# Kernel tuning notes

Hardware: AMD Instinct MI355X
Metric: run time of the kernel (lower is better)

Reference implementation:

```python
import jax, jax.numpy as jnp
import numpy as np

MLOG32 = float(np.log(32.0))


def _maxpool(x, k):
    # F.max_pool2d(stride=1, padding=k//2) pads with -inf, matching init value
    pad = k // 2
    return jax.lax.reduce_window(x, -jnp.inf, jax.lax.max, (1, 1, k, k), (1, 1, 1, 1),
                                 ((0, 0), (0, 0), (pad, pad), (pad, pad)))


def _minpool(x, k):
    return -_maxpool(-x, k)


def _local_sum(x, k):
    # conv2d with all-ones kxk kernel, zero padding, same spatial size
    pad = k // 2
    return jax.lax.reduce_window(x, 0.0, jax.lax.add, (1, 1, k, k), (1, 1, 1, 1),
                                 ((0, 0), (0, 0), (pad, pad), (pad, pad)))


def _conv3(x, kern):
    # torch conv2d == cross-correlation == lax conv (no kernel flip)
    return jax.lax.conv_general_dilated(x, kern, (1, 1), ((1, 1), (1, 1)),
                                        dimension_numbers=('NCHW', 'OIHW', 'NCHW'))


def _otsu(gray, bins=32):
    # vectorized per-batch Otsu threshold; gray in [0,1]
    B, _, H, W = gray.shape
    v = gray.reshape(B, -1)
    idx = jnp.clip((v * bins).astype(jnp.int32), 0, bins - 1)  # histc semantics, v==1 -> last bin
    hist = jax.vmap(lambda i: jnp.bincount(i, length=bins))(idx).astype(gray.dtype)
    p = hist / (H * W + 1e-6)
    xs = jnp.linspace(0.0, 1.0, bins, dtype=gray.dtype)
    omega = jnp.cumsum(p, axis=1)
    mu = jnp.cumsum(p * xs[None, :], axis=1)
    mu_t = mu[:, -1:]
    sigma_b2 = (mu_t * omega - mu) ** 2 / (omega * (1.0 - omega) + 1e-8)
    kbest = jnp.argmax(sigma_b2, axis=1)
    edges = jnp.linspace(0.0, 1.0, bins + 1, dtype=gray.dtype)
    return edges[kbest].reshape(B, 1, 1, 1)


def _concept_maps(image_rgb, cell_dilate=10, k_local=9):
    r, g, b = image_rgb[:, 0:1], image_rgb[:, 1:2], image_rgb[:, 2:3]
    gray = jnp.clip(0.5 * (0.299 * r + 0.587 * g + 0.114 * b + 1.0), 0.0, 1.0)
    thr = _otsu(gray)
    nuc = (gray <= thr).astype(gray.dtype)
    # morphological open+close, k=3
    e = _minpool(nuc, 3)
    d = _maxpool(e, 3)
    d = _maxpool(d, 3)
    e2 = _minpool(d, 3)
    nuc = (e2 > 0.5).astype(gray.dtype)
    er = _minpool(nuc, 3)
    boundary = jnp.maximum(nuc - er, 0.0)
    lap_k = jnp.array([[0, 1, 0], [1, -4, 1], [0, 1, 0]], dtype=gray.dtype).reshape(1, 1, 3, 3)
    lap = jnp.abs(_conv3(nuc, lap_k))
    den = _local_sum(boundary, 5) + 1e-6
    roughness = lap * boundary / den
    kx = jnp.array([[1, 0, -1], [2, 0, -2], [1, 0, -1]], dtype=gray.dtype).reshape(1, 1, 3, 3)
    ky = jnp.array([[1, 2, 1], [0, 0, 0], [-1, -2, -1]], dtype=gray.dtype).reshape(1, 1, 3, 3)
    gx = _conv3(gray, kx)
    gy = _conv3(gray, ky)
    ang = jnp.arctan2(gy, gx)
    den_orient = _local_sum(jnp.ones_like(gray), k_local) + 1e-6
    ms = _local_sum(jnp.sin(ang), k_local) / den_orient
    mc = _local_sum(jnp.cos(ang), k_local) / den_orient
    circ_var = 1.0 - jnp.sqrt(ms ** 2 + mc ** 2 + 1e-6)
    kd = cell_dilate if cell_dilate % 2 == 1 else cell_dilate + 1  # force odd
    cell = jnp.minimum(_maxpool(nuc, kd), 1.0)
    A_n = _local_sum(nuc, k_local)
    A_c = jnp.maximum(_local_sum(cell, k_local) - A_n, 1.0)
    nc = A_n / A_c
    g2 = _local_sum(gray * gray, k_local) / den_orient
    g1 = _local_sum(gray, k_local) / den_orient
    ent_like = jnp.log1p(jnp.maximum(g2 - g1 * g1, 0.0))
    z_maps = jnp.concatenate([roughness, circ_var, nc, ent_like], axis=1)
    return z_maps, nuc


def _energy_forward(image_rgb, cal_a, cal_b, alpha_logits, tau_p, Ht, Wt):
    z_maps, nuc = _concept_maps(image_rgb)
    z0 = jnp.log1p(jnp.maximum(z_maps[:, 0:1], 0.0))
    z1 = jnp.clip(z_maps[:, 1:2], 0.0, 1.0)
    z2 = jnp.log1p(jnp.maximum(z_maps[:, 2:3], 0.0))
    z3 = jnp.clip(z_maps[:, 3:4], 0.0, MLOG32)
    z_stable = jnp.concatenate([z0, z1, z2, z3], axis=1)
    z_cal = jax.nn.softplus(cal_a)[None, :, None, None] * z_stable + cal_b[None, :, None, None]
    alpha = jax.nn.softmax(alpha_logits)[None, :, None, None]
    E = jnp.sum(alpha * z_cal, axis=1, keepdims=True)
    B = E.shape[0]
    if (E.shape[2], E.shape[3]) != (Ht, Wt):
        E_t = jax.image.resize(E, (B, 1, Ht, Wt), method='linear')
    else:
        E_t = E
    tau = 0.2 + jax.nn.softplus(tau_p)
    A = jax.nn.softmax((-E_t / tau).reshape(B, 1, Ht * Wt), axis=-1).reshape(B, 1, Ht, Wt)
    return A, z_maps, nuc, E_t


def setup_inputs() -> dict:
    key = jax.random.key(0)
    k1, k2, k3, k4 = jax.random.split(key, 4)
    B, H, W = 16, 512, 512
    image_rgb = 2.0 * jax.random.uniform(k1, (B, 3, H, W), dtype=jnp.float32) - 1.0
    cal_a = 1.0 + 0.1 * jax.random.normal(k2, (4,), jnp.float32)
    cal_b = 0.1 * jax.random.normal(k3, (4,), jnp.float32)
    alpha_logits = 0.1 * jax.random.normal(k4, (4,), jnp.float32)
    tau_p = jnp.float32(0.5)
    return {"image_rgb": image_rgb, "cal_a": cal_a, "cal_b": cal_b,
            "alpha_logits": alpha_logits, "tau_p": tau_p, "target_h": 512, "target_w": 512}


def reference(image_rgb, cal_a, cal_b, alpha_logits, tau_p, target_h, target_w):
    return _energy_forward(image_rgb, cal_a, cal_b, alpha_logits, tau_p, int(target_h), int(target_w))
```

## Files before the change

kernel.cpp:

```cpp
#include <hip/hip_runtime.h>
#include <math.h>
#include <stdint.h>

#define HW 512
#define IMG (HW*HW)
#define GS 49
#define MLOG32f 3.4657359027997265f
#define WFENCE() __asm__ __volatile__("" ::: "memory")

__device__ __forceinline__ float grayf(float r, float g, float b) {
    float t = __fadd_rn(__fadd_rn(__fmul_rn(0.299f, r), __fmul_rn(0.587f, g)), __fmul_rn(0.114f, b));
    float s = __fmul_rn(0.5f, __fadd_rn(t, 1.0f));
    return fminf(fmaxf(s, 0.0f), 1.0f);
}

__device__ __forceinline__ float softplusf(float x) {
    return fmaxf(x, 0.0f) + log1pf(expf(-fabsf(x)));
}

__device__ __forceinline__ float frcp(float x)  { return __builtin_amdgcn_rcpf(x); }
__device__ __forceinline__ float frsq(float x)  { return __builtin_amdgcn_rsqf(x); }
__device__ __forceinline__ float flog1p(float x){ return __logf(1.0f + x); }

__device__ __forceinline__ uint64_t kmask(int lo, int hi) {
    return (1ull << hi) - (1ull << lo);
}

__global__ __launch_bounds__(256) void k_gray_hist(const float* __restrict__ img,
                                                   float* __restrict__ gray,
                                                   int* __restrict__ hist) {
    __shared__ int lh[32];
    int tid = threadIdx.x;
    int b = blockIdx.y;
    if (tid < 32) lh[tid] = 0;
    __syncthreads();
    const float4* rp = (const float4*)(img + (size_t)b * 3 * IMG);
    const float4* gp = (const float4*)(img + (size_t)b * 3 * IMG + IMG);
    const float4* bp = (const float4*)(img + (size_t)b * 3 * IMG + 2 * IMG);
    float4* op = (float4*)(gray + (size_t)b * IMG);
    int i = blockIdx.x * 256 + tid;
    float4 r = rp[i], g = gp[i], bb = bp[i];
    float4 o;
    o.x = grayf(r.x, g.x, bb.x);
    o.y = grayf(r.y, g.y, bb.y);
    o.z = grayf(r.z, g.z, bb.z);
    o.w = grayf(r.w, g.w, bb.w);
    op[i] = o;
    int idx[4];
    idx[0] = min(max((int)(o.x * 32.0f), 0), 31);
    idx[1] = min(max((int)(o.y * 32.0f), 0), 31);
    idx[2] = min(max((int)(o.z * 32.0f), 0), 31);
    idx[3] = min(max((int)(o.w * 32.0f), 0), 31);
    int lane = tid & 63;
    int bin = lane & 31;
    int cnt = 0;
    #pragma unroll
    for (int e = 0; e < 4; e++) {
        int v = idx[e];
        unsigned long long m0 = __ballot((v & 1)  != 0);
        unsigned long long m1 = __ballot((v & 2)  != 0);
        unsigned long long m2 = __ballot((v & 4)  != 0);
        unsigned long long m3 = __ballot((v & 8)  != 0);
        unsigned long long m4 = __ballot((v & 16) != 0);
        unsigned long long mm = (bin & 1)  ? m0 : ~m0;
        mm &= (bin & 2)  ? m1 : ~m1;
        mm &= (bin & 4)  ? m2 : ~m2;
        mm &= (bin & 8)  ? m3 : ~m3;
        mm &= (bin & 16) ? m4 : ~m4;
        cnt += __popcll(mm);
    }
    if (lane < 32) atomicAdd(&lh[bin], cnt);
    __syncthreads();
    if (tid < 32) atomicAdd(&hist[b * 32 + tid], lh[tid]);
}

__global__ void k_otsu_sc(const int* __restrict__ hist,
                          const float* __restrict__ cal_a, const float* __restrict__ cal_b,
                          const float* __restrict__ alpha_logits, const float* __restrict__ tau_p,
                          float* __restrict__ thr, float* __restrict__ sc, int B) {
    int tid = threadIdx.x;
    if (tid < B) {
        const int* h = hist + tid * 32;
        float omega[32], mu[32];
        float co = 0.0f, cm = 0.0f;
        for (int k = 0; k < 32; k++) {
            float pk = (float)h[k] * (1.0f / 262144.0f);
            float xs = (float)((double)k / 31.0);
            co += pk;
            cm += pk * xs;
            omega[k] = co; mu[k] = cm;
        }
        float mu_t = mu[31];
        float best = -1e30f; int kb = 0;
        for (int k = 0; k < 32; k++) {
            float t = mu_t * omega[k] - mu[k];
            float sb = (t * t) / (omega[k] * (1.0f - omega[k]) + 1e-8f);
            if (sb > best) { best = sb; kb = k; }
        }
        thr[tid] = (float)kb * 0.03125f;
    }
    if (tid == 63) {
        float al[4];
        float m = -1e30f;
        for (int c = 0; c < 4; c++) { al[c] = alpha_logits[c]; m = fmaxf(m, al[c]); }
        float e[4]; float s = 0.0f;
        for (int c = 0; c < 4; c++) { e[c] = expf(al[c] - m); s += e[c]; }
        float bias = 0.0f;
        for (int c = 0; c < 4; c++) {
            float alpha = e[c] / s;
            sc[c] = alpha * softplusf(cal_a[c]);
            bias += alpha * cal_b[c];
        }
        sc[4] = bias;
        float tau = 0.2f + softplusf(tau_p[0]);
        sc[5] = tau;
        sc[6] = -1.0f / tau;
    }
}

__global__ __launch_bounds__(256) void k_thresh(const float* __restrict__ gray,
                                                const float* __restrict__ thr,
                                                uint32_t* __restrict__ packed) {
    int b = blockIdx.y;
    int i = blockIdx.x * 256 + threadIdx.x;
    float t = thr[b];
    float v = gray[(size_t)b * IMG + i];
    unsigned long long m = __ballot(v <= t);
    if ((threadIdx.x & 63) == 0)
        *(uint64_t*)&packed[(size_t)b * 8192 + (i >> 5)] = m;
}

__global__ __launch_bounds__(256, 5) void k_maps(const float* __restrict__ gray,
                                              const uint32_t* __restrict__ p0,
                                              float* __restrict__ zmap,
                                              float* __restrict__ nucf,
                                              float* __restrict__ Eout,
                                              const float* __restrict__ sc,
                                              float* __restrict__ expsum) {
    __shared__ __align__(16) char smem[30248];
    float*    gt   = (float*)smem;
    float2*   rsP1 = (float2*)(smem + 8232);
    float2*   rsP2 = (float2*)(smem + 18728);
    uint64_t* m0   = (uint64_t*)(smem + 8232);
    uint64_t* m1   = m0 + 58;
    uint64_t* dilh = m1 + 58;
    uint64_t* ehr  = dilh + 50;
    uint64_t* nrow = (uint64_t*)(smem + 29224);
    uint64_t* bnd  = nrow + 50;
    uint64_t* cell = bnd + 36;
    int*      rs_nPT = (int*)smem;
    int*      rs_cPT = (int*)(smem + 1408);
    int*      rs_bPT = (int*)(smem + 2816);
    float*    red  = (float*)(smem + 30232);

    int tid = threadIdx.x, b = blockIdx.z;
    int x0 = blockIdx.x * 32, y0 = blockIdx.y * 32;
    int w0 = x0 >> 5;
    const float* gb = gray + (size_t)b * IMG;
    const uint32_t* pb = p0 + (size_t)b * 8192;

    if (tid >= 64) {
        for (int s = tid - 64; s < 504; s += 192) {
            int r = s / 12, c4 = s - r * 12;
            int gy = y0 + r - 5;
            int gxf = (x0 >> 2) + c4 - 2;
            float4 v = make_float4(0.f, 0.f, 0.f, 0.f);
            if ((unsigned)gy < (unsigned)HW && (unsigned)gxf < 128u)
                v = *(const float4*)(gb + gy * HW + (gxf << 2));
            float* dst = &gt[r * GS + (c4 << 2)];
            dst[0] = v.x; dst[1] = v.y; dst[2] = v.z; dst[3] = v.w;
        }
    } else {
        int ml = tid;
        uint64_t mcol = ~0ull;
        if (x0 == 0)   mcol &= ~((1ull << 13) - 1);
        if (x0 == 480) mcol = (1ull << 45) - 1;
        if (ml < 58) {
            int gy = y0 - 13 + ml;
            uint64_t v = 0;
            if ((unsigned)gy < (unsigned)HW) {
                const uint32_t* rowp = pb + gy * 16;
                uint64_t wm = (w0 > 0)  ? rowp[w0 - 1] : 0;
                uint64_t wc = rowp[w0];
                uint64_t wp = (w0 < 15) ? rowp[w0 + 1] : 0;
                v = (wm >> 19) | (wc << 13) | (wp << 45);
            }
            m0[ml] = v;
        }
        WFENCE();
        if (ml >= 1 && ml < 57) {
            uint64_t e = ~0ull;
            #pragma unroll
            for (int dt = -1; dt <= 1; dt++) {
                int q = ml + dt;
                int gy = y0 - 13 + q;
                uint64_t vv = ((unsigned)gy < (unsigned)HW) ? (m0[q] | ~mcol) : ~0ull;
                e &= vv & (vv << 1) & (vv >> 1);
            }
            m1[ml] = e;
        }
        WFENCE();
        if (ml >= 2 && ml < 56) {
            uint64_t d = 0;
            #pragma unroll
            for (int dt = -1; dt <= 1; dt++) {
                int q = ml + dt;
                int gy = y0 - 13 + q;
                uint64_t vv = ((unsigned)gy < (unsigned)HW) ? (m1[q] & mcol) : 0;
                d |= vv | (vv << 1) | (vv >> 1);
            }
            m0[ml] = d;
        }
        WFENCE();
        if (ml >= 3 && ml < 55) {
            uint64_t d = 0;
            #pragma unroll
            for (int dt = -1; dt <= 1; dt++) {
                int q = ml + dt;
                int gy = y0 - 13 + q;
                uint64_t vv = ((unsigned)gy < (unsigned)HW) ? (m0[q] & mcol) : 0;
                d |= vv | (vv << 1) | (vv >> 1);
            }
            m1[ml] = d;
        }
        WFENCE();
        if (ml >= 4 && ml < 54) {
            uint64_t e = ~0ull;
            #pragma unroll
            for (int dt = -1; dt <= 1; dt++) {
                int q = ml + dt;
                int gy = y0 - 13 + q;
                uint64_t vv = ((unsigned)gy < (unsigned)HW) ? (m1[q] | ~mcol) : ~0ull;
                e &= vv & (vv << 1) & (vv >> 1);
            }
            m0[ml] = e;
        }
        WFENCE();
        if (ml < 50) {
            int gy = y0 - 9 + ml;
            uint64_t v = 0;
            if ((unsigned)gy < (unsigned)HW)
                v = ((m0[ml + 4] & mcol) >> 4) & ((1ull << 50) - 1);
            nrow[ml] = v;
        }
        WFENCE();
        uint64_t mwin = kmask(x0 == 0 ? 9 : 0, x0 == 480 ? 41 : 50);
        if (ml < 50) {
            uint64_t v = nrow[ml];
            uint64_t d = v | (v << 1) | (v >> 1);
            d = d | (d << 2) | (d >> 2);
            d = d | (d << 2) | (d >> 2);
            dilh[ml] = d;
        }
        if (ml >= 6 && ml < 44) {
            int y = y0 - 9 + ml;
            uint64_t m = ((unsigned)y < (unsigned)HW) ? mwin : 0;
            uint64_t v = nrow[ml] | ~m;
            ehr[ml] = v & (v << 1) & (v >> 1);
        }
        WFENCE();
        if (ml < 36) {
            int r = ml + 7;
            uint64_t er = ehr[r - 1] & ehr[r] & ehr[r + 1];
            bnd[ml] = nrow[r] & ~er;
        }
        if (ml < 40) {
            int r = ml + 5;
            int y = y0 - 4 + ml;
            uint64_t c = 0;
            #pragma unroll
            for (int d = -5; d <= 5; d++) c |= dilh[r + d];
            uint64_t m = ((unsigned)y < (unsigned)HW) ? mwin : 0;
            cell[ml] = c & m;
        }
    }
    __syncthreads();

    for (int i = tid; i < 320; i += 256) {
        int ly = i >> 3, c0 = (i & 7) << 2;
        int gyb = y0 + ly - 4;
        bool rowok = (unsigned)gyb < (unsigned)HW;
        int gx0 = x0 + c0 - 4;
        int base = ly * GS + c0 + 3;
        float a0p = gt[base],          a1p = gt[base + GS],          a2p = gt[base + 2 * GS];
        float a0q = gt[base + 1],      a1q = gt[base + GS + 1],      a2q = gt[base + 2 * GS + 1];
        float sa[12], ca[12], v[12];
        #pragma unroll
        for (int j = 0; j < 12; j++) {
            float a0r = gt[base + 2 + j], a1r = gt[base + GS + 2 + j], a2r = gt[base + 2 * GS + 2 + j];
            v[j] = a1q;
            float s = 0.0f, c = 0.0f;
            if (rowok && (unsigned)(gx0 + j) < (unsigned)HW) {
                float gxv = (a0p - a0r) + 2.0f * (a1p - a1r) + (a2p - a2r);
                float gyv = (a0p + 2.0f * a0q + a0r) - (a2p + 2.0f * a2q + a2r);
                float r2 = gxv * gxv + gyv * gyv;
                if (r2 > 0.0f) { float ir = frsq(r2); s = gyv * ir; c = gxv * ir; }
                else { s = 0.0f; c = 1.0f; }
            }
            sa[j] = s; ca[j] = c;
            a0p = a0q; a1p = a1q; a2p = a2q;
            a0q = a0r; a1q = a1r; a2q = a2r;
        }
        float ss = sa[0]+sa[1]+sa[2]+sa[3]+sa[4]+sa[5]+sa[6]+sa[7]+sa[8];
        float cs = ca[0]+ca[1]+ca[2]+ca[3]+ca[4]+ca[5]+ca[6]+ca[7]+ca[8];
        float gs = v[0]+v[1]+v[2]+v[3]+v[4]+v[5]+v[6]+v[7]+v[8];
        float g2 = v[0]*v[0]+v[1]*v[1]+v[2]*v[2]+v[3]*v[3]+v[4]*v[4]+v[5]*v[5]+v[6]*v[6]+v[7]*v[7]+v[8]*v[8];
        #pragma unroll
        for (int q = 0; q < 4; q++) {
            float2 t1; t1.x = ss; t1.y = cs;
            float2 t2; t2.x = gs; t2.y = g2;
            rsP1[(c0 + q) * 41 + ly] = t1;
            rsP2[(c0 + q) * 41 + ly] = t2;
            if (q < 3) {
                ss += sa[9 + q] - sa[q]; cs += ca[9 + q] - ca[q];
                gs += v[9 + q] - v[q];
                g2 += v[9 + q] * v[9 + q] - v[q] * v[q];
            }
        }
    }
    __syncthreads();

    int p = tid & 31, py0 = (tid >> 5) << 2;
    int gx = x0 + p;
    float cntx = (float)(min(gx + 4, HW - 1) - max(gx - 4, 0) + 1);
    float z1v[4], z3v[4];
    {
        float2 v[12];
        #pragma unroll
        for (int j = 0; j < 12; j++) v[j] = rsP1[p * 41 + py0 + j];
        float ss = v[0].x+v[1].x+v[2].x+v[3].x+v[4].x+v[5].x+v[6].x+v[7].x+v[8].x;
        float cs = v[0].y+v[1].y+v[2].y+v[3].y+v[4].y+v[5].y+v[6].y+v[7].y+v[8].y;
        #pragma unroll
        for (int q = 0; q < 4; q++) {
            int gy = y0 + py0 + q;
            float cnty = (float)(min(gy + 4, HW - 1) - max(gy - 4, 0) + 1);
            float iden = frcp(cnty * cntx + 1e-6f);
            float ms = ss * iden, mc = cs * iden;
            z1v[q] = 1.0f - sqrtf(ms * ms + mc * mc + 1e-6f);
            if (q < 3) { ss += v[9 + q].x - v[q].x; cs += v[9 + q].y - v[q].y; }
        }
    }
    {
        float2 v[12];
        #pragma unroll
        for (int j = 0; j < 12; j++) v[j] = rsP2[p * 41 + py0 + j];
        float gs = v[0].x+v[1].x+v[2].x+v[3].x+v[4].x+v[5].x+v[6].x+v[7].x+v[8].x;
        float g2 = v[0].y+v[1].y+v[2].y+v[3].y+v[4].y+v[5].y+v[6].y+v[7].y+v[8].y;
        #pragma unroll
        for (int q = 0; q < 4; q++) {
            int gy = y0 + py0 + q;
            float cnty = (float)(min(gy + 4, HW - 1) - max(gy - 4, 0) + 1);
            float iden = frcp(cnty * cntx + 1e-6f);
            float g1 = gs * iden, gq = g2 * iden;
            z3v[q] = flog1p(fmaxf(gq - g1 * g1, 0.0f));
            if (q < 3) { gs += v[9 + q].x - v[q].x; g2 += v[9 + q].y - v[q].y; }
        }
    }
    for (int i = tid; i < 320; i += 256) {
        int rr = i >> 3, p8 = i & 7, pbase = p8 << 2;
        uint64_t rn = nrow[rr + 5], rc = cell[rr];
        int vn = 0, vc = 0;
        #pragma unroll
        for (int e = 0; e < 4; e++) {
            int pp = pbase + e;
            vn |= __popcll((rn >> (pp + 5)) & 0x1FFull) << (e * 8);
            vc |= __popcll((rc >> (pp + 5)) & 0x1FFull) << (e * 8);
        }
        rs_nPT[p8 * 44 + rr] = vn;
        rs_cPT[p8 * 44 + rr] = vc;
    }
    for (int i = tid; i < 288; i += 256) {
        int rr = i >> 3, p8 = i & 7, pbase = p8 << 2;
        uint64_t rb = bnd[rr];
        int vb = 0;
        #pragma unroll
        for (int e = 0; e < 4; e++) {
            int pp = pbase + e;
            vb |= __popcll((rb >> (pp + 7)) & 0x1Full) << (e * 8);
        }
        rs_bPT[p8 * 40 + rr] = vb;
    }
    __syncthreads();

    float w0f = sc[0], w1f = sc[1], w2f = sc[2], w3f = sc[3], bias = sc[4], ntau = sc[6];
    float* z0p = zmap + ((size_t)b * 4 + 0) * IMG;
    float* z1p = zmap + ((size_t)b * 4 + 1) * IMG;
    float* z2p = zmap + ((size_t)b * 4 + 2) * IMG;
    float* z3p = zmap + ((size_t)b * 4 + 3) * IMG;
    float* Ep  = Eout + (size_t)b * IMG;
    float* np  = nucf + (size_t)b * IMG;
    float acc = 0.0f;
    {
        int p8 = p >> 2, sh = (p & 3) << 3;
        int4 na = *(const int4*)&rs_nPT[p8 * 44 + py0];
        int4 nb = *(const int4*)&rs_nPT[p8 * 44 + py0 + 4];
        int4 nc = *(const int4*)&rs_nPT[p8 * 44 + py0 + 8];
        int4 ka = *(const int4*)&rs_cPT[p8 * 44 + py0];
        int4 kb = *(const int4*)&rs_cPT[p8 * 44 + py0 + 4];
        int4 kc = *(const int4*)&rs_cPT[p8 * 44 + py0 + 8];
        int4 ba = *(const int4*)&rs_bPT[p8 * 40 + py0];
        int4 bbv = *(const int4*)&rs_bPT[p8 * 40 + py0 + 4];
        int en[12], ec[12], eb[8];
        en[0]=na.x; en[1]=na.y; en[2]=na.z; en[3]=na.w;
        en[4]=nb.x; en[5]=nb.y; en[6]=nb.z; en[7]=nb.w;
        en[8]=nc.x; en[9]=nc.y; en[10]=nc.z; en[11]=nc.w;
        ec[0]=ka.x; ec[1]=ka.y; ec[2]=ka.z; ec[3]=ka.w;
        ec[4]=kb.x; ec[5]=kb.y; ec[6]=kb.z; ec[7]=kb.w;
        ec[8]=kc.x; ec[9]=kc.y; ec[10]=kc.z; ec[11]=kc.w;
        eb[0]=ba.x; eb[1]=ba.y; eb[2]=ba.z; eb[3]=ba.w;
        eb[4]=bbv.x; eb[5]=bbv.y; eb[6]=bbv.z; eb[7]=bbv.w;
        #pragma unroll
        for (int j = 0; j < 12; j++) { en[j] = (en[j] >> sh) & 0xFF; ec[j] = (ec[j] >> sh) & 0xFF; }
        #pragma unroll
        for (int j = 0; j < 8; j++) eb[j] = (eb[j] >> sh) & 0xFF;
        int An = en[0]+en[1]+en[2]+en[3]+en[4]+en[5]+en[6]+en[7]+en[8];
        int Ac = ec[0]+ec[1]+ec[2]+ec[3]+ec[4]+ec[5]+ec[6]+ec[7]+ec[8];
        int db = eb[0]+eb[1]+eb[2]+eb[3]+eb[4];
        int kk = p + 9;
        #pragma unroll
        for (int q = 0; q < 4; q++) {
            int py = py0 + q;
            int r = py + 9;
            uint64_t rowc = nrow[r];
            int cbit = (int)((rowc >> kk) & 1);
            int nb4  = (int)((nrow[r - 1] >> kk) & 1) + (int)((nrow[r + 1] >> kk) & 1)
                     + (int)((rowc >> (kk - 1)) & 1) + (int)((rowc >> (kk + 1)) & 1);
            int lap = nb4 - 4 * cbit; lap = lap < 0 ? -lap : lap;
            int bc  = (int)((bnd[py + 2] >> kk) & 1);
            float rough = (float)(lap * bc) * frcp((float)db + 1e-6f);
            float z2 = (float)An * frcp(fmaxf((float)(Ac - An), 1.0f));
            float z0s = flog1p(fmaxf(rough, 0.0f));
            float z1s = fminf(fmaxf(z1v[q], 0.0f), 1.0f);
            float z2s = flog1p(fmaxf(z2, 0.0f));
            float z3s = fminf(fmaxf(z3v[q], 0.0f), MLOG32f);
            float E = w0f * z0s + w1f * z1s + w2f * z2s + w3f * z3s + bias;
            int gy = y0 + py;
            size_t o = (size_t)gy * HW + x0 + p;
            z0p[o] = rough;
            z1p[o] = z1v[q];
            z2p[o] = z2;
            z3p[o] = z3v[q];
            Ep[o]  = E;
            np[o]  = (float)cbit;
            acc += __expf(E * ntau);
            if (q < 3) {
                An += en[9 + q] - en[q];
                Ac += ec[9 + q] - ec[q];
                db += eb[5 + q] - eb[q];
            }
        }
    }
    for (int off = 32; off > 0; off >>= 1) acc += __shfl_down(acc, off, 64);
    if ((tid & 63) == 0) red[tid >> 6] = acc;
    __syncthreads();
    if (tid == 0) atomicAdd(&expsum[b], red[0] + red[1] + red[2] + red[3]);
}

__global__ __launch_bounds__(256) void k_softmaxA(const float* __restrict__ E,
                                                  float* __restrict__ A,
                                                  const float* __restrict__ sc,
                                                  const float* __restrict__ expsum) {
    int b = blockIdx.y;
    int i = blockIdx.x * 256 + threadIdx.x;
    float ntau = sc[6];
    float invS = 1.0f / expsum[b];
    const float4* Ep = (const float4*)(E + (size_t)b * IMG);
    float4* Ap = (float4*)(A + (size_t)b * IMG);
    float4 e = Ep[i];
    float4 o;
    o.x = __expf(e.x * ntau) * invS;
    o.y = __expf(e.y * ntau) * invS;
    o.z = __expf(e.z * ntau) * invS;
    o.w = __expf(e.w * ntau) * invS;
    Ap[i] = o;
}

extern "C" void kernel_launch(void* const* d_in, const int* in_sizes, int n_in,
                              void* d_out, int out_size, void* d_ws, size_t ws_size,
                              hipStream_t stream) {
    const float* img   = (const float*)d_in[0];
    const float* cal_a = (const float*)d_in[1];
    const float* cal_b = (const float*)d_in[2];
    const float* alpha = (const float*)d_in[3];
    const float* tau_p = (const float*)d_in[4];
    int B = in_sizes[0] / (3 * IMG);

    float* out  = (float*)d_out;
    float* A    = out;
    float* zmap = out + (size_t)B * IMG;
    float* nuc  = out + (size_t)B * IMG * 5;
    float* E    = out + (size_t)B * IMG * 6;
    float* gray = A;

    int*      hist    = (int*)d_ws;
    float*    expsum  = (float*)d_ws + B * 32;
    float*    thr     = expsum + B;
    float*    sc      = thr + B;
    uint32_t* packed0 = (uint32_t*)d_ws + 1024;

    hipMemsetAsync(d_ws, 0, (size_t)(B * 32 + B) * 4, stream);
    k_gray_hist<<<dim3(IMG / 1024, B), 256, 0, stream>>>(img, gray, hist);
    k_otsu_sc<<<1, 64, 0, stream>>>(hist, cal_a, cal_b, alpha, tau_p, thr, sc, B);
    k_thresh<<<dim3(IMG / 256, B), 256, 0, stream>>>(gray, thr, packed0);
    dim3 tg(HW / 32, HW / 32, B);
    k_maps<<<tg, 256, 0, stream>>>(gray, packed0, zmap, nuc, E, sc, expsum);
    k_softmaxA<<<dim3(IMG / 1024, B), 256, 0, stream>>>(E, A, sc, expsum);
}
```

Baseline: 240.0 us.

## Shrink k_maps shared memory by aliasing buffers and computing popcounts per thread

The Sobel pass now keeps the gray-sum partials in registers and writes them to a buffer that aliases the gray tile once a barrier has passed, which cuts the shared-memory footprint. The packed popcount tables in shared memory are replaced by per-thread popcount computation straight from the bitmask rows, removing a pass and a barrier. Launch bounds rise from 5 to 7 blocks per SM to take advantage of the lower LDS use. The cost is an extra barrier, more registers held across it, and redundant popcount work per thread.

```diff
diff --git a/kernel.cpp b/kernel.cpp
--- a/kernel.cpp
+++ b/kernel.cpp
@@ -130,28 +130,69 @@
         *(uint64_t*)&packed[(size_t)b * 8192 + (i >> 5)] = m;
 }
 
-__global__ __launch_bounds__(256, 5) void k_maps(const float* __restrict__ gray,
+__device__ __forceinline__ void sobel_item(const float* __restrict__ gt, float2* __restrict__ rsP1,
+                                           int i, int x0, int y0,
+                                           float* __restrict__ hgs, float* __restrict__ hg2) {
+    int ly = i >> 3, c0 = (i & 7) << 2;
+    int gyb = y0 + ly - 4;
+    bool rowok = (unsigned)gyb < (unsigned)HW;
+    int gx0 = x0 + c0 - 4;
+    int base = ly * GS + c0 + 3;
+    float a0p = gt[base],          a1p = gt[base + GS],          a2p = gt[base + 2 * GS];
+    float a0q = gt[base + 1],      a1q = gt[base + GS + 1],      a2q = gt[base + 2 * GS + 1];
+    float sa[12], ca[12], v[12];
+    #pragma unroll
+    for (int j = 0; j < 12; j++) {
+        float a0r = gt[base + 2 + j], a1r = gt[base + GS + 2 + j], a2r = gt[base + 2 * GS + 2 + j];
+        v[j] = a1q;
+        float s = 0.0f, c = 0.0f;
+        if (rowok && (unsigned)(gx0 + j) < (unsigned)HW) {
+            float gxv = (a0p - a0r) + 2.0f * (a1p - a1r) + (a2p - a2r);
+            float gyv = (a0p + 2.0f * a0q + a0r) - (a2p + 2.0f * a2q + a2r);
+            float r2 = gxv * gxv + gyv * gyv;
+            if (r2 > 0.0f) { float ir = frsq(r2); s = gyv * ir; c = gxv * ir; }
+            else { s = 0.0f; c = 1.0f; }
+        }
+        sa[j] = s; ca[j] = c;
+        a0p = a0q; a1p = a1q; a2p = a2q;
+        a0q = a0r; a1q = a1r; a2q = a2r;
+    }
+    float ss = sa[0]+sa[1]+sa[2]+sa[3]+sa[4]+sa[5]+sa[6]+sa[7]+sa[8];
+    float cs = ca[0]+ca[1]+ca[2]+ca[3]+ca[4]+ca[5]+ca[6]+ca[7]+ca[8];
+    float gs = v[0]+v[1]+v[2]+v[3]+v[4]+v[5]+v[6]+v[7]+v[8];
+    float g2 = v[0]*v[0]+v[1]*v[1]+v[2]*v[2]+v[3]*v[3]+v[4]*v[4]+v[5]*v[5]+v[6]*v[6]+v[7]*v[7]+v[8]*v[8];
+    #pragma unroll
+    for (int q = 0; q < 4; q++) {
+        float2 t1; t1.x = ss; t1.y = cs;
+        rsP1[(c0 + q) * 41 + ly] = t1;
+        hgs[q] = gs; hg2[q] = g2;
+        if (q < 3) {
+            ss += sa[9 + q] - sa[q]; cs += ca[9 + q] - ca[q];
+            gs += v[9 + q] - v[q];
+            g2 += v[9 + q] * v[9 + q] - v[q] * v[q];
+        }
+    }
+}
+
+__global__ __launch_bounds__(256, 7) void k_maps(const float* __restrict__ gray,
                                               const uint32_t* __restrict__ p0,
                                               float* __restrict__ zmap,
                                               float* __restrict__ nucf,
                                               float* __restrict__ Eout,
                                               const float* __restrict__ sc,
                                               float* __restrict__ expsum) {
-    __shared__ __align__(16) char smem[30248];
+    __shared__ __align__(16) char smem[22016];
     float*    gt   = (float*)smem;
-    float2*   rsP1 = (float2*)(smem + 8232);
-    float2*   rsP2 = (float2*)(smem + 18728);
-    uint64_t* m0   = (uint64_t*)(smem + 8232);
+    float2*   rsP2 = (float2*)smem;
+    float2*   rsP1 = (float2*)(smem + 10496);
+    uint64_t* m0   = (uint64_t*)(smem + 10496);
     uint64_t* m1   = m0 + 58;
     uint64_t* dilh = m1 + 58;
     uint64_t* ehr  = dilh + 50;
-    uint64_t* nrow = (uint64_t*)(smem + 29224);
+    uint64_t* nrow = (uint64_t*)(smem + 20992);
     uint64_t* bnd  = nrow + 50;
     uint64_t* cell = bnd + 36;
-    int*      rs_nPT = (int*)smem;
-    int*      rs_cPT = (int*)(smem + 1408);
-    int*      rs_bPT = (int*)(smem + 2816);
-    float*    red  = (float*)(smem + 30232);
+    float*    red  = (float*)(smem + 22000);
 
     int tid = threadIdx.x, b = blockIdx.z;
     int x0 = blockIdx.x * 32, y0 = blockIdx.y * 32;
@@ -276,46 +317,25 @@
     }
     __syncthreads();
 
-    for (int i = tid; i < 320; i += 256) {
-        int ly = i >> 3, c0 = (i & 7) << 2;
-        int gyb = y0 + ly - 4;
-        bool rowok = (unsigned)gyb < (unsigned)HW;
-        int gx0 = x0 + c0 - 4;
-        int base = ly * GS + c0 + 3;
-        float a0p = gt[base],          a1p = gt[base + GS],          a2p = gt[base + 2 * GS];
-        float a0q = gt[base + 1],      a1q = gt[base + GS + 1],      a2q = gt[base + 2 * GS + 1];
-        float sa[12], ca[12], v[12];
-        #pragma unroll
-        for (int j = 0; j < 12; j++) {
-            float a0r = gt[base + 2 + j], a1r = gt[base + GS + 2 + j], a2r = gt[base + 2 * GS + 2 + j];
-            v[j] = a1q;
-            float s = 0.0f, c = 0.0f;
-            if (rowok && (unsigned)(gx0 + j) < (unsigned)HW) {
-                float gxv = (a0p - a0r) + 2.0f * (a1p - a1r) + (a2p - a2r);
-                float gyv = (a0p + 2.0f * a0q + a0r) - (a2p + 2.0f * a2q + a2r);
-                float r2 = gxv * gxv + gyv * gyv;
-                if (r2 > 0.0f) { float ir = frsq(r2); s = gyv * ir; c = gxv * ir; }
-                else { s = 0.0f; c = 1.0f; }
-            }
-            sa[j] = s; ca[j] = c;
-            a0p = a0q; a1p = a1q; a2p = a2q;
-            a0q = a0r; a1q = a1r; a2q = a2r;
-        }
-        float ss = sa[0]+sa[1]+sa[2]+sa[3]+sa[4]+sa[5]+sa[6]+sa[7]+sa[8];
-        float cs = ca[0]+ca[1]+ca[2]+ca[3]+ca[4]+ca[5]+ca[6]+ca[7]+ca[8];
-        float gs = v[0]+v[1]+v[2]+v[3]+v[4]+v[5]+v[6]+v[7]+v[8];
-        float g2 = v[0]*v[0]+v[1]*v[1]+v[2]*v[2]+v[3]*v[3]+v[4]*v[4]+v[5]*v[5]+v[6]*v[6]+v[7]*v[7]+v[8]*v[8];
+    float hgs0[4], hg20[4], hgs1[4], hg21[4];
+    sobel_item(gt, rsP1, tid, x0, y0, hgs0, hg20);
+    if (tid < 64) sobel_item(gt, rsP1, tid + 256, x0, y0, hgs1, hg21);
+    __syncthreads();
+
+    {
+        int ly = tid >> 3, c0 = (tid & 7) << 2;
         #pragma unroll
         for (int q = 0; q < 4; q++) {
-            float2 t1; t1.x = ss; t1.y = cs;
-            float2 t2; t2.x = gs; t2.y = g2;
-            rsP1[(c0 + q) * 41 + ly] = t1;
-            rsP2[(c0 + q) * 41 + ly] = t2;
-            if (q < 3) {
-                ss += sa[9 + q] - sa[q]; cs += ca[9 + q] - ca[q];
-                gs += v[9 + q] - v[q];
-                g2 += v[9 + q] * v[9 + q] - v[q] * v[q];
-            }
+            float2 t; t.x = hgs0[q]; t.y = hg20[q];
+            rsP2[(c0 + q) * 41 + ly] = t;
+        }
+    }
+    if (tid < 64) {
+        int i = tid + 256; int ly = i >> 3, c0 = (i & 7) << 2;
+        #pragma unroll
+        for (int q = 0; q < 4; q++) {
+            float2 t; t.x = hgs1[q]; t.y = hg21[q];
+            rsP2[(c0 + q) * 41 + ly] = t;
         }
     }
     __syncthreads();
@@ -356,31 +376,15 @@
             if (q < 3) { gs += v[9 + q].x - v[q].x; g2 += v[9 + q].y - v[q].y; }
         }
     }
-    for (int i = tid; i < 320; i += 256) {
-        int rr = i >> 3, p8 = i & 7, pbase = p8 << 2;
-        uint64_t rn = nrow[rr + 5], rc = cell[rr];
-        int vn = 0, vc = 0;
-        #pragma unroll
-        for (int e = 0; e < 4; e++) {
-            int pp = pbase + e;
-            vn |= __popcll((rn >> (pp + 5)) & 0x1FFull) << (e * 8);
-            vc |= __popcll((rc >> (pp + 5)) & 0x1FFull) << (e * 8);
-        }
-        rs_nPT[p8 * 44 + rr] = vn;
-        rs_cPT[p8 * 44 + rr] = vc;
-    }
-    for (int i = tid; i < 288; i += 256) {
-        int rr = i >> 3, p8 = i & 7, pbase = p8 << 2;
-        uint64_t rb = bnd[rr];
-        int vb = 0;
-        #pragma unroll
-        for (int e = 0; e < 4; e++) {
-            int pp = pbase + e;
-            vb |= __popcll((rb >> (pp + 7)) & 0x1Full) << (e * 8);
-        }
-        rs_bPT[p8 * 40 + rr] = vb;
-    }
-    __syncthreads();
+    int pn[12], pcc[12], pbv[8];
+    #pragma unroll
+    for (int j = 0; j < 12; j++) {
+        pn[j]  = (int)__popcll((nrow[py0 + 5 + j] >> (p + 5)) & 0x1FFull);
+        pcc[j] = (int)__popcll((cell[py0 + j]     >> (p + 5)) & 0x1FFull);
+    }
+    #pragma unroll
+    for (int j = 0; j < 8; j++)
+        pbv[j] = (int)__popcll((bnd[py0 + j] >> (p + 7)) & 0x1Full);
 
     float w0f = sc[0], w1f = sc[1], w2f = sc[2], w3f = sc[3], bias = sc[4], ntau = sc[6];
     float* z0p = zmap + ((size_t)b * 4 + 0) * IMG;
@@ -391,31 +395,9 @@
     float* np  = nucf + (size_t)b * IMG;
     float acc = 0.0f;
     {
-        int p8 = p >> 2, sh = (p & 3) << 3;
-        int4 na = *(const int4*)&rs_nPT[p8 * 44 + py0];
-        int4 nb = *(const int4*)&rs_nPT[p8 * 44 + py0 + 4];
-        int4 nc = *(const int4*)&rs_nPT[p8 * 44 + py0 + 8];
-        int4 ka = *(const int4*)&rs_cPT[p8 * 44 + py0];
-        int4 kb = *(const int4*)&rs_cPT[p8 * 44 + py0 + 4];
-        int4 kc = *(const int4*)&rs_cPT[p8 * 44 + py0 + 8];
-        int4 ba = *(const int4*)&rs_bPT[p8 * 40 + py0];
-        int4 bbv = *(const int4*)&rs_bPT[p8 * 40 + py0 + 4];
-        int en[12], ec[12], eb[8];
-        en[0]=na.x; en[1]=na.y; en[2]=na.z; en[3]=na.w;
-        en[4]=nb.x; en[5]=nb.y; en[6]=nb.z; en[7]=nb.w;
-        en[8]=nc.x; en[9]=nc.y; en[10]=nc.z; en[11]=nc.w;
-        ec[0]=ka.x; ec[1]=ka.y; ec[2]=ka.z; ec[3]=ka.w;
-        ec[4]=kb.x; ec[5]=kb.y; ec[6]=kb.z; ec[7]=kb.w;
-        ec[8]=kc.x; ec[9]=kc.y; ec[10]=kc.z; ec[11]=kc.w;
-        eb[0]=ba.x; eb[1]=ba.y; eb[2]=ba.z; eb[3]=ba.w;
-        eb[4]=bbv.x; eb[5]=bbv.y; eb[6]=bbv.z; eb[7]=bbv.w;
-        #pragma unroll
-        for (int j = 0; j < 12; j++) { en[j] = (en[j] >> sh) & 0xFF; ec[j] = (ec[j] >> sh) & 0xFF; }
-        #pragma unroll
-        for (int j = 0; j < 8; j++) eb[j] = (eb[j] >> sh) & 0xFF;
-        int An = en[0]+en[1]+en[2]+en[3]+en[4]+en[5]+en[6]+en[7]+en[8];
-        int Ac = ec[0]+ec[1]+ec[2]+ec[3]+ec[4]+ec[5]+ec[6]+ec[7]+ec[8];
-        int db = eb[0]+eb[1]+eb[2]+eb[3]+eb[4];
+        int An = pn[0]+pn[1]+pn[2]+pn[3]+pn[4]+pn[5]+pn[6]+pn[7]+pn[8];
+        int Ac = pcc[0]+pcc[1]+pcc[2]+pcc[3]+pcc[4]+pcc[5]+pcc[6]+pcc[7]+pcc[8];
+        int db = pbv[0]+pbv[1]+pbv[2]+pbv[3]+pbv[4];
         int kk = p + 9;
         #pragma unroll
         for (int q = 0; q < 4; q++) {
@@ -444,9 +426,9 @@
             np[o]  = (float)cbit;
             acc += __expf(E * ntau);
             if (q < 3) {
-                An += en[9 + q] - en[q];
-                Ac += ec[9 + q] - ec[q];
-                db += eb[5 + q] - eb[q];
+                An += pn[9 + q] - pn[q];
+                Ac += pcc[9 + q] - pcc[q];
+                db += pbv[5 + q] - pbv[q];
             }
         }
     }
```

New measurement: 261.6 us. +9.0%, slower.
